# Kernel optimization log

Hardware: AMD Instinct MI355X
Metric: run time of the kernel (lower is better)

Reference implementation:

```python
import jax, jax.numpy as jnp
import numpy as np

N, E, B = 100000, 800000, 64
IN, HC1, HC2, NC, SA = 256, 128, 32, 2, 350
NEG = 0.2  # GATv2Conv default negative_slope


def forward(s_x, s_edge_index, s_batch, s_root_n_id,
            Wq, bq, Wk, bk, Wv, bv,
            Wl1, bl1, Wr1, br1, att1, bias1,
            Wl2, bl2, Wr2, br2, att2, bias2,
            Wl3, bl3, Wr3, br3, att3, bias3,
            c1w, c1b, c2W, c2b, c3W, c3b,
            linW, linb, aW1, ab1, aW2, mW1, mb1, mW2, mb2):
    src, dst = s_edge_index[0], s_edge_index[1]
    x_info = s_x
    # --- SelfAttention over seq_len=1 (x.unsqueeze(1)) ---
    z = s_x[:, None, :]                                   # [N,1,IN]
    q = z @ Wq + bq; k = z @ Wk + bk; v = z @ Wv + bv      # [N,1,SA]
    scores = jnp.einsum('nqd,nkd->nqk', q, k) / jnp.sqrt(jnp.float32(SA))
    probs = jax.nn.softmax(scores, axis=-1)
    h = jnp.einsum('nqk,nkd->nqd', probs, v)[:, 0, :]      # [N,SA]

    def gatv2(x, Wl, bl, Wr, br, att, bias):
        # PyG GATv2Conv, heads=1, eval mode (dropout off)
        xl = x @ Wl + bl                                   # source transform [N,O]
        xr = x @ Wr + br                                   # target transform [N,O]
        e = jax.nn.leaky_relu(xl[src] + xr[dst], NEG)      # [E,O]
        s = e @ att                                        # [E]
        smax = jax.ops.segment_max(s, dst, num_segments=N)
        smax = jnp.where(jnp.isfinite(smax), smax, 0.0)
        ex = jnp.exp(s - smax[dst])
        den = jax.ops.segment_sum(ex, dst, num_segments=N)
        alpha = ex / jnp.maximum(den[dst], 1e-16)
        return jax.ops.segment_sum(alpha[:, None] * xl[src], dst, num_segments=N) + bias

    h = jax.nn.relu(gatv2(h, Wl1, bl1, Wr1, br1, att1, bias1))
    h = jax.nn.relu(gatv2(h, Wl2, bl2, Wr2, br2, att2, bias2))
    h = jax.nn.relu(gatv2(h, Wl3, bl3, Wr3, br3, att3, bias3))   # [N,HC2]

    # --- readout: root node feature ++ global mean pool ---
    cnt = jax.ops.segment_sum(jnp.ones((N,), h.dtype), s_batch, num_segments=B)
    pooled = jax.ops.segment_sum(h, s_batch, num_segments=B) / jnp.maximum(cnt, 1.0)[:, None]
    sx = jnp.concatenate([h[s_root_n_id], pooled], axis=-1)       # [B,2*HC2]

    # --- info branch on raw root features ---
    info = x_info[s_root_n_id]                                    # [B,IN]
    info = c1w[0] * info[:, :-2] + c1w[1] * info[:, 1:-1] + c1w[2] * info[:, 2:] + c1b  # Conv1d(1,1,3)
    t = info.T                                                    # [IN-2,B]
    t = jax.nn.relu(c2W @ t + c2b[:, None])                       # [HC1,B]
    t = jax.nn.relu(c3W @ t + c3b[:, None])                       # [HC1//2,B]
    t = t.T                                                       # [B,HC1//2]
    L = t.shape[1]
    t = jax.nn.relu(t.reshape(B, HC2, L // HC2).mean(-1))         # AdaptiveAvgPool1d(HC2)

    sx = jax.nn.relu(sx @ linW + linb)                            # [B,HC2]

    # --- semantic attention over the two views ---
    emb = jnp.stack([sx, t], axis=1)                              # [B,2,HC2]
    w = jnp.tanh(emb @ aW1 + ab1) @ aW2                           # [B,2,1]
    beta = jax.nn.softmax(w, axis=1)
    emb = (beta * emb).sum(1)                                     # [B,HC2]

    return jax.nn.softmax(jnp.tanh(emb @ mW1 + mb1) @ mW2 + mb2, axis=1)  # [B,NC]


def setup_inputs() -> dict:
    keys = iter(jax.random.split(jax.random.key(0), 64))
    def nrm(*shape):
        return jax.random.normal(next(keys), shape, dtype=jnp.float32) * 0.05
    inp = {}
    inp['s_x'] = jax.random.normal(next(keys), (N, IN), dtype=jnp.float32)
    inp['s_edge_index'] = jax.random.randint(next(keys), (2, E), 0, N)
    inp['s_batch'] = jnp.sort(jax.random.randint(next(keys), (N,), 0, B))
    inp['s_root_n_id'] = jax.random.randint(next(keys), (B,), 0, N)
    inp['Wq'] = nrm(IN, SA); inp['bq'] = nrm(SA)
    inp['Wk'] = nrm(IN, SA); inp['bk'] = nrm(SA)
    inp['Wv'] = nrm(IN, SA); inp['bv'] = nrm(SA)
    inp['Wl1'] = nrm(SA, HC1); inp['bl1'] = nrm(HC1)
    inp['Wr1'] = nrm(SA, HC1); inp['br1'] = nrm(HC1)
    inp['att1'] = nrm(HC1); inp['bias1'] = nrm(HC1)
    inp['Wl2'] = nrm(HC1, HC1 // 2); inp['bl2'] = nrm(HC1 // 2)
    inp['Wr2'] = nrm(HC1, HC1 // 2); inp['br2'] = nrm(HC1 // 2)
    inp['att2'] = nrm(HC1 // 2); inp['bias2'] = nrm(HC1 // 2)
    inp['Wl3'] = nrm(HC1 // 2, HC2); inp['bl3'] = nrm(HC2)
    inp['Wr3'] = nrm(HC1 // 2, HC2); inp['br3'] = nrm(HC2)
    inp['att3'] = nrm(HC2); inp['bias3'] = nrm(HC2)
    inp['c1w'] = nrm(3); inp['c1b'] = nrm(1)
    inp['c2W'] = nrm(HC1, IN - 2); inp['c2b'] = nrm(HC1)
    inp['c3W'] = nrm(HC1 // 2, HC1); inp['c3b'] = nrm(HC1 // 2)
    inp['linW'] = nrm(2 * HC2, HC2); inp['linb'] = nrm(HC2)
    inp['aW1'] = nrm(HC2, 16); inp['ab1'] = nrm(16); inp['aW2'] = nrm(16, 1)
    inp['mW1'] = nrm(HC2, 16); inp['mb1'] = nrm(16)
    inp['mW2'] = nrm(16, NC); inp['mb2'] = nrm(NC)
    return inp


def reference(s_x, s_edge_index, s_batch, s_root_n_id,
              Wq, bq, Wk, bk, Wv, bv,
              Wl1, bl1, Wr1, br1, att1, bias1,
              Wl2, bl2, Wr2, br2, att2, bias2,
              Wl3, bl3, Wr3, br3, att3, bias3,
              c1w, c1b, c2W, c2b, c3W, c3b,
              linW, linb, aW1, ab1, aW2, mW1, mb1, mW2, mb2):
    return forward(s_x, s_edge_index, s_batch, s_root_n_id,
                   Wq, bq, Wk, bk, Wv, bv,
                   Wl1, bl1, Wr1, br1, att1, bias1,
                   Wl2, bl2, Wr2, br2, att2, bias2,
                   Wl3, bl3, Wr3, br3, att3, bias3,
                   c1w, c1b, c2W, c2b, c3W, c3b,
                   linW, linb, aW1, ab1, aW2, mW1, mb1, mW2, mb2)
```

## Files before the change

### kernel.cpp

```cpp
#include <hip/hip_runtime.h>
#include <hip/hip_bf16.h>
#include <math.h>

typedef unsigned short ushort_t;
typedef __attribute__((ext_vector_type(8))) short bfrag;
typedef __attribute__((ext_vector_type(4))) float ffrag;

constexpr int N_NODES = 100000;
constexpr int N_EDGES = 800000;
constexpr int NB      = 64;
constexpr int IN_F    = 256;
constexpr int HC1C    = 128;
constexpr int HC2C    = 32;
constexpr int SA_D    = 350;
constexpr float NEG   = 0.2f;

constexpr int SCAN_NBLK = (N_NODES + 255) / 256;
constexpr int MB128     = (N_NODES + 127) / 128;

constexpr size_t OFF_WT1    = 0;
constexpr size_t OFF_WT2    = OFF_WT1 + 65536;
constexpr size_t OFF_WT3    = OFF_WT2 + 16384;
constexpr size_t OFF_BC1    = OFF_WT3 + 4096;
constexpr size_t OFF_BC2    = OFF_BC1 + 256;
constexpr size_t OFF_BC3    = OFF_BC2 + 128;
constexpr size_t OFF_XLR    = OFF_BC3 + 64;
constexpr size_t OFF_H      = OFF_XLR + (size_t)N_NODES * 256;
constexpr size_t OFF_DEG    = OFF_H + (size_t)N_NODES * 128;
constexpr size_t OFF_ROWPTR = OFF_DEG + N_NODES;
constexpr size_t OFF_CURSOR = OFF_ROWPTR + N_NODES + 1;
constexpr size_t OFF_BLKS   = OFF_CURSOR + N_NODES;
constexpr size_t OFF_BLKO   = OFF_BLKS + 512;
constexpr size_t OFF_CSRSRC = OFF_BLKO + 512;
constexpr size_t OFF_POOLED = OFF_CSRSRC + N_EDGES;
constexpr size_t OFF_CNT    = OFF_POOLED + NB * HC2C;
constexpr size_t WS_FLOATS  = OFF_CNT + NB;

__device__ __forceinline__ ushort_t f2bf(float f) {
  union { float f; unsigned int u; } a;
  a.f = f;
  unsigned int r = a.u + 0x7FFFu + ((a.u >> 16) & 1u);
  return (ushort_t)(r >> 16);
}
__device__ __forceinline__ float bf2f(ushort_t h) {
  union { unsigned int u; float f; } a;
  a.u = ((unsigned int)h) << 16;
  return a.f;
}
__device__ __forceinline__ float2 bfp(unsigned int u) {
  float2 r;
  r.x = __uint_as_float(u << 16);
  r.y = __uint_as_float(u & 0xFFFF0000u);
  return r;
}
__device__ __forceinline__ unsigned int pack2(float a, float b) {
  unsigned int ua = __float_as_uint(a);
  ua += 0x7FFFu + ((ua >> 16) & 1u);
  unsigned int ub = __float_as_uint(b);
  ub += 0x7FFFu + ((ub >> 16) & 1u);
  return __builtin_amdgcn_perm(ub, ua, 0x07060302u);
}
__device__ __forceinline__ void unp8(uint4 u, float* x) {
  float2 p0 = bfp(u.x), p1 = bfp(u.y), p2 = bfp(u.z), p3 = bfp(u.w);
  x[0] = p0.x; x[1] = p0.y; x[2] = p1.x; x[3] = p1.y;
  x[4] = p2.x; x[5] = p2.y; x[6] = p3.x; x[7] = p3.y;
}

__global__ void k_pack_all(const float* __restrict__ Wv, const float* __restrict__ bv,
                           const float* __restrict__ Wl1, const float* __restrict__ bl1,
                           const float* __restrict__ Wr1, const float* __restrict__ br1,
                           const float* __restrict__ Wl2, const float* __restrict__ bl2,
                           const float* __restrict__ Wr2, const float* __restrict__ br2,
                           const float* __restrict__ Wl3, const float* __restrict__ bl3,
                           const float* __restrict__ Wr3, const float* __restrict__ br3,
                           ushort_t* __restrict__ WT1, float* __restrict__ bc1,
                           ushort_t* __restrict__ WT2, float* __restrict__ bc2,
                           ushort_t* __restrict__ WT3, float* __restrict__ bc3) {
  int blk = blockIdx.x;
  int tid = threadIdx.x;
  if (blk < 256) {
    int t = blk * 256 + tid;
    int n = t & 255, k = t >> 8;
    const float* Wx = (n < 128) ? Wl1 : Wr1;
    int j = n & 127;
    float a = 0.f;
    for (int kk = 0; kk < SA_D; ++kk) a += Wv[k * SA_D + kk] * Wx[kk * 128 + j];
    WT1[(size_t)n * 256 + k] = f2bf(a);
  } else if (blk == 256) {
    int n = tid;
    const float* Wx = (n < 128) ? Wl1 : Wr1;
    const float* bx = (n < 128) ? bl1 : br1;
    int j = n & 127;
    float a = bx[j];
    for (int kk = 0; kk < SA_D; ++kk) a += bv[kk] * Wx[kk * 128 + j];
    bc1[n] = a;
  } else if (blk < 321) {
    int t = (blk - 257) * 256 + tid;
    int n = t & 127, k = t >> 7;
    if (t < 128) bc2[t] = (t < 64) ? bl2[t] : br2[t - 64];
    float v = (n < 64) ? Wl2[k * 64 + n] : Wr2[k * 64 + (n - 64)];
    WT2[(size_t)n * 128 + k] = f2bf(v);
  } else {
    int t = (blk - 321) * 256 + tid;
    int n = t & 63, k = t >> 6;
    if (t < 64) bc3[t] = (t < 32) ? bl3[t] : br3[t - 32];
    float v = (n < 32) ? Wl3[k * 32 + n] : Wr3[k * 32 + (n - 32)];
    WT3[(size_t)n * 64 + k] = f2bf(v);
  }
}

__global__ void k_hist(const int* __restrict__ dst, int* __restrict__ deg) {
  int e = blockIdx.x * blockDim.x + threadIdx.x;
  if (e < N_EDGES) atomicAdd(deg + dst[e], 1);
}

__global__ void k_scan_local(const int* __restrict__ deg, int* __restrict__ row_ptr,
                             int* __restrict__ blk_sum) {
  __shared__ int sh[256];
  int t = threadIdx.x;
  int i = blockIdx.x * 256 + t;
  int v = (i < N_NODES) ? deg[i] : 0;
  sh[t] = v;
  __syncthreads();
  for (int off = 1; off < 256; off <<= 1) {
    int add = (t >= off) ? sh[t - off] : 0;
    __syncthreads();
    sh[t] += add;
    __syncthreads();
  }
  if (i < N_NODES) row_ptr[i] = sh[t] - v;
  if (t == 255) blk_sum[blockIdx.x] = sh[255];
}

__global__ void k_scan_blk(const int* __restrict__ blk_sum, int* __restrict__ blk_off) {
  __shared__ int sh[512];
  int t = threadIdx.x;
  int v = (t < SCAN_NBLK) ? blk_sum[t] : 0;
  sh[t] = v;
  __syncthreads();
  for (int off = 1; off < 512; off <<= 1) {
    int add = (t >= off) ? sh[t - off] : 0;
    __syncthreads();
    sh[t] += add;
    __syncthreads();
  }
  blk_off[t] = sh[t] - v;
}

__global__ void k_scan_add(int* __restrict__ row_ptr, const int* __restrict__ blk_off,
                           int* __restrict__ cursor) {
  int i = blockIdx.x * blockDim.x + threadIdx.x;
  if (i < N_NODES) {
    int v = row_ptr[i] + blk_off[i >> 8];
    row_ptr[i] = v;
    cursor[i] = v;
  }
  if (i == 0) row_ptr[N_NODES] = N_EDGES;
}

__global__ void k_fill(const int* __restrict__ src, const int* __restrict__ dst,
                       int* __restrict__ cursor, int* __restrict__ csr_src) {
  int e = blockIdx.x * blockDim.x + threadIdx.x;
  if (e >= N_EDGES) return;
  int pos = atomicAdd(cursor + dst[e], 1);
  csr_src[pos] = src[e];
}

template <int K, int NN, int BN, bool AF32>
__global__ __launch_bounds__(256) void k_gemm_bf16(const void* __restrict__ xin,
                                                   const ushort_t* __restrict__ WT,
                                                   const float* __restrict__ bc,
                                                   ushort_t* __restrict__ out, int M) {
  constexpr int BM  = 128;
  constexpr int RT  = 2;
  constexpr int CT  = BN / 16;
  constexpr int NK  = K / 32;
  constexpr int CPR = K / 8;
  __shared__ ushort_t Bs[(size_t)BN * K];

  const int tid  = threadIdx.x;
  const int wave = tid >> 6;
  const int lane = tid & 63;
  const int quad = lane >> 4;
  const int l16  = lane & 15;
  const int x7   = l16 & 7;
  const int m0   = blockIdx.x * BM;
  const int n0   = blockIdx.y * BN;

  constexpr int NCHUNK = BN * CPR;
  static_assert(NCHUNK % 256 == 0, "staging divisibility");
#pragma unroll
  for (int it = 0; it < NCHUNK / 256; ++it) {
    unsigned idx = it * 256u + tid;
    unsigned n  = idx / CPR;
    unsigned cp = idx % CPR;
    unsigned c  = cp ^ (n & 7u);
    uint4 u = *(const uint4*)(WT + (size_t)(n0 + n) * K + c * 8);
    *(uint4*)&Bs[(size_t)idx * 8] = u;
  }
  __syncthreads();

  const float*    af32 = (const float*)xin;
  const ushort_t* ab16 = (const ushort_t*)xin;
  size_t aoff[RT];
#pragma unroll
  for (int rt = 0; rt < RT; ++rt) {
    int m = m0 + wave * 32 + rt * 16 + l16;
    if (m >= M) m = M - 1;
    aoff[rt] = (size_t)m * K + quad * 8;
  }

  ffrag acc[RT][CT];
#pragma unroll
  for (int rt = 0; rt < RT; ++rt)
#pragma unroll
    for (int ct = 0; ct < CT; ++ct) acc[rt][ct] = ffrag{0.f, 0.f, 0.f, 0.f};

  float4 pf0[RT], pf1[RT];
  bfrag  pb[RT];
  if (AF32) {
#pragma unroll
    for (int rt = 0; rt < RT; ++rt) {
      pf0[rt] = *(const float4*)(af32 + aoff[rt]);
      pf1[rt] = *(const float4*)(af32 + aoff[rt] + 4);
    }
  } else {
#pragma unroll
    for (int rt = 0; rt < RT; ++rt) pb[rt] = *(const bfrag*)(ab16 + aoff[rt]);
  }

#pragma unroll
  for (int ks = 0; ks < NK; ++ks) {
    bfrag a[RT];
    if (AF32) {
#pragma unroll
      for (int rt = 0; rt < RT; ++rt) {
        uint4 d;
        d.x = pack2(pf0[rt].x, pf0[rt].y);
        d.y = pack2(pf0[rt].z, pf0[rt].w);
        d.z = pack2(pf1[rt].x, pf1[rt].y);
        d.w = pack2(pf1[rt].z, pf1[rt].w);
        a[rt] = *(bfrag*)&d;
      }
    } else {
#pragma unroll
      for (int rt = 0; rt < RT; ++rt) a[rt] = pb[rt];
    }
    if (ks + 1 < NK) {
      if (AF32) {
#pragma unroll
        for (int rt = 0; rt < RT; ++rt) {
          pf0[rt] = *(const float4*)(af32 + aoff[rt] + (ks + 1) * 32);
          pf1[rt] = *(const float4*)(af32 + aoff[rt] + (ks + 1) * 32 + 4);
        }
      } else {
#pragma unroll
        for (int rt = 0; rt < RT; ++rt)
          pb[rt] = *(const bfrag*)(ab16 + aoff[rt] + (ks + 1) * 32);
      }
    }
#pragma unroll
    for (int ct = 0; ct < CT; ++ct) {
      const int cc = (ks * 4 + quad) ^ x7;
      bfrag b = *(const bfrag*)&Bs[(size_t)(ct * 16 + l16) * K + cc * 8];
#pragma unroll
      for (int rt = 0; rt < RT; ++rt)
        acc[rt][ct] = __builtin_amdgcn_mfma_f32_16x16x32_bf16(a[rt], b, acc[rt][ct], 0, 0, 0);
    }
  }

#pragma unroll
  for (int rt = 0; rt < RT; ++rt)
#pragma unroll
    for (int ct = 0; ct < CT; ++ct) {
      const int n = n0 + ct * 16 + l16;
      const float bb = bc[n];
#pragma unroll
      for (int r = 0; r < 4; ++r) {
        const int m = m0 + wave * 32 + rt * 16 + quad * 4 + r;
        if (m < M) out[(size_t)m * NN + n] = f2bf(acc[rt][ct][r] + bb);
      }
    }
}

template <int C>
__global__ void k_gat(const ushort_t* __restrict__ xlr, const int* __restrict__ row_ptr,
                      const int* __restrict__ csr_src, const float* __restrict__ att,
                      const float* __restrict__ bias, ushort_t* __restrict__ h) {
  constexpr int G = C / 8;
  constexpr int RS = 2 * C;
  int t = blockIdx.x * blockDim.x + threadIdx.x;
  int d = t / G;
  int lane = t - d * G;
  if (d >= N_NODES) return;
  float xr[8], a[8];
  unp8(*(const uint4*)(xlr + (size_t)d * RS + C + lane * 8), xr);
  *(float4*)&a[0] = *(const float4*)(att + lane * 8);
  *(float4*)&a[4] = *(const float4*)(att + lane * 8 + 4);
  float acc[8];
#pragma unroll
  for (int j = 0; j < 8; ++j) acc[j] = 0.f;
  float den = 0.f;
  const int e0 = row_ptr[d], e1 = row_ptr[d + 1];
  int i = e0;
  for (; i + 4 <= e1; i += 4) {
    uint4 u[4];
#pragma unroll
    for (int q = 0; q < 4; ++q)
      u[q] = *(const uint4*)(xlr + (size_t)csr_src[i + q] * RS + lane * 8);
    float xl[4][8];
#pragma unroll
    for (int q = 0; q < 4; ++q) unp8(u[q], xl[q]);
    float p[4] = {0.f, 0.f, 0.f, 0.f};
#pragma unroll
    for (int j = 0; j < 8; ++j) {
#pragma unroll
      for (int q = 0; q < 4; ++q) {
        float v = xl[q][j] + xr[j];
        v = v > 0.f ? v : NEG * v;
        p[q] += a[j] * v;
      }
    }
#pragma unroll
    for (int off = G / 2; off > 0; off >>= 1) {
#pragma unroll
      for (int q = 0; q < 4; ++q) p[q] += __shfl_xor(p[q], off, 64);
    }
    float ex[4];
#pragma unroll
    for (int q = 0; q < 4; ++q) ex[q] = expf(p[q]);
    den += (ex[0] + ex[1]) + (ex[2] + ex[3]);
#pragma unroll
    for (int j = 0; j < 8; ++j)
      acc[j] += (ex[0] * xl[0][j] + ex[1] * xl[1][j]) + (ex[2] * xl[2][j] + ex[3] * xl[3][j]);
  }
  for (; i < e1; ++i) {
    int s = csr_src[i];
    float xl[8];
    unp8(*(const uint4*)(xlr + (size_t)s * RS + lane * 8), xl);
    float p = 0.f;
#pragma unroll
    for (int j = 0; j < 8; ++j) {
      float v = xl[j] + xr[j];
      v = v > 0.f ? v : NEG * v;
      p += a[j] * v;
    }
#pragma unroll
    for (int off = G / 2; off > 0; off >>= 1) p += __shfl_xor(p, off, 64);
    float ex = expf(p);
    den += ex;
#pragma unroll
    for (int j = 0; j < 8; ++j) acc[j] += ex * xl[j];
  }
  float inv = 1.f / fmaxf(den, 1e-16f);
  float o[8];
#pragma unroll
  for (int j = 0; j < 8; ++j)
    o[j] = fmaxf(acc[j] * inv + bias[lane * 8 + j], 0.f);
  uint4 pk;
  pk.x = pack2(o[0], o[1]);
  pk.y = pack2(o[2], o[3]);
  pk.z = pack2(o[4], o[5]);
  pk.w = pack2(o[6], o[7]);
  *(uint4*)(h + (size_t)d * C + lane * 8) = pk;
}

__global__ void k_pool(const ushort_t* __restrict__ h3, const int* __restrict__ batch,
                       float* __restrict__ pooled, float* __restrict__ cnt) {
  constexpr int NPB = 1024;
  constexpr int NPT = NPB / 8;
  int c = threadIdx.x & 31;
  int r = threadIdx.x >> 5;
  int base = blockIdx.x * NPB + r * NPT;
  if (base >= N_NODES) return;
  int end = base + NPT;
  if (end > N_NODES) end = N_NODES;
  int cur_b = batch[base];
  float acc = 0.f, count = 0.f;
  for (int n = base; n < end; ++n) {
    int b = batch[n];
    if (b != cur_b) {
      atomicAdd(pooled + cur_b * HC2C + c, acc);
      if (c == 0) atomicAdd(cnt + cur_b, count);
      cur_b = b;
      acc = 0.f;
      count = 0.f;
    }
    acc += bf2f(h3[(size_t)n * HC2C + c]);
    count += 1.f;
  }
  atomicAdd(pooled + cur_b * HC2C + c, acc);
  if (c == 0) atomicAdd(cnt + cur_b, count);
}

__global__ __launch_bounds__(256) void k_tail(
    const ushort_t* __restrict__ h3, const int* __restrict__ root,
    const float* __restrict__ pooled, const float* __restrict__ cnt,
    const float* __restrict__ linW, const float* __restrict__ linb,
    const float* __restrict__ X, const float* __restrict__ c1w,
    const float* __restrict__ c1b, const float* __restrict__ c2W,
    const float* __restrict__ c2b, const float* __restrict__ c3W,
    const float* __restrict__ c3b, const float* __restrict__ aW1,
    const float* __restrict__ ab1, const float* __restrict__ aW2,
    const float* __restrict__ mW1, const float* __restrict__ mb1,
    const float* __restrict__ mW2, const float* __restrict__ mb2,
    float* __restrict__ out) {
  constexpr int L = IN_F - 2;
  __shared__ float s_info[L];
  __shared__ float s_t1[HC1C];
  __shared__ float s_t2[HC1C / 2];
  __shared__ float s_e0[HC2C];
  __shared__ float s_e1[HC2C];
  const int b = blockIdx.x;
  const int tid = threadIdx.x;
  const int r = root[b];
  const float* xr = X + (size_t)r * IN_F;
  for (int i = tid; i < L; i += 256)
    s_info[i] = c1w[0] * xr[i] + c1w[1] * xr[i + 1] + c1w[2] * xr[i + 2] + c1b[0];
  __syncthreads();
  if (tid < HC1C) {
    float a = c2b[tid];
    for (int i = 0; i < L; ++i) a += c2W[tid * L + i] * s_info[i];
    s_t1[tid] = fmaxf(a, 0.f);
  }
  __syncthreads();
  if (tid < HC1C / 2) {
    float a = c3b[tid];
    for (int i = 0; i < HC1C; ++i) a += c3W[tid * HC1C + i] * s_t1[i];
    s_t2[tid] = fmaxf(a, 0.f);
  }
  __syncthreads();
  if (tid < HC2C) {
    float v = 0.5f * (s_t2[2 * tid] + s_t2[2 * tid + 1]);
    s_e1[tid] = fmaxf(v, 0.f);
  } else if (tid < 2 * HC2C) {
    int j = tid - HC2C;
    float inv = 1.f / fmaxf(cnt[b], 1.f);
    float a = linb[j];
    for (int c = 0; c < HC2C; ++c) a += bf2f(h3[(size_t)r * HC2C + c]) * linW[c * HC2C + j];
    for (int c = 0; c < HC2C; ++c) a += pooled[b * HC2C + c] * inv * linW[(HC2C + c) * HC2C + j];
    s_e0[j] = fmaxf(a, 0.f);
  }
  __syncthreads();
  if (tid == 0) {
    float w0 = 0.f, w1 = 0.f;
    for (int j = 0; j < 16; ++j) {
      float z0 = ab1[j], z1 = ab1[j];
      for (int c = 0; c < HC2C; ++c) {
        z0 += s_e0[c] * aW1[c * 16 + j];
        z1 += s_e1[c] * aW1[c * 16 + j];
      }
      w0 += tanhf(z0) * aW2[j];
      w1 += tanhf(z1) * aW2[j];
    }
    float mx = fmaxf(w0, w1);
    float x0 = expf(w0 - mx), x1 = expf(w1 - mx);
    float inv = 1.f / (x0 + x1);
    float b0 = x0 * inv, b1 = x1 * inv;
    float l0 = mb2[0], l1 = mb2[1];
    for (int j = 0; j < 16; ++j) {
      float z = mb1[j];
      for (int c = 0; c < HC2C; ++c) z += (b0 * s_e0[c] + b1 * s_e1[c]) * mW1[c * 16 + j];
      float tz = tanhf(z);
      l0 += tz * mW2[j * 2 + 0];
      l1 += tz * mW2[j * 2 + 1];
    }
    float m2 = fmaxf(l0, l1);
    float y0 = expf(l0 - m2), y1 = expf(l1 - m2);
    float is = 1.f / (y0 + y1);
    out[b * 2 + 0] = y0 * is;
    out[b * 2 + 1] = y1 * is;
  }
}

extern "C" void kernel_launch(void* const* d_in, const int* in_sizes, int n_in, void* d_out,
                              int out_size, void* d_ws, size_t ws_size, hipStream_t stream) {
  if (ws_size < WS_FLOATS * sizeof(float)) return;

  const float* s_x   = (const float*)d_in[0];
  const int*   edge  = (const int*)d_in[1];
  const int*   batch = (const int*)d_in[2];
  const int*   root  = (const int*)d_in[3];
  const float* Wv    = (const float*)d_in[8];
  const float* bv    = (const float*)d_in[9];
  const float* Wl1   = (const float*)d_in[10];
  const float* bl1   = (const float*)d_in[11];
  const float* Wr1   = (const float*)d_in[12];
  const float* br1   = (const float*)d_in[13];
  const float* att1  = (const float*)d_in[14];
  const float* bias1 = (const float*)d_in[15];
  const float* Wl2   = (const float*)d_in[16];
  const float* bl2   = (const float*)d_in[17];
  const float* Wr2   = (const float*)d_in[18];
  const float* br2   = (const float*)d_in[19];
  const float* att2  = (const float*)d_in[20];
  const float* bias2 = (const float*)d_in[21];
  const float* Wl3   = (const float*)d_in[22];
  const float* bl3   = (const float*)d_in[23];
  const float* Wr3   = (const float*)d_in[24];
  const float* br3   = (const float*)d_in[25];
  const float* att3  = (const float*)d_in[26];
  const float* bias3 = (const float*)d_in[27];
  const float* c1w   = (const float*)d_in[28];
  const float* c1b   = (const float*)d_in[29];
  const float* c2W   = (const float*)d_in[30];
  const float* c2b   = (const float*)d_in[31];
  const float* c3W   = (const float*)d_in[32];
  const float* c3b   = (const float*)d_in[33];
  const float* linW  = (const float*)d_in[34];
  const float* linb  = (const float*)d_in[35];
  const float* aW1   = (const float*)d_in[36];
  const float* ab1   = (const float*)d_in[37];
  const float* aW2   = (const float*)d_in[38];
  const float* mW1   = (const float*)d_in[39];
  const float* mb1   = (const float*)d_in[40];
  const float* mW2   = (const float*)d_in[41];
  const float* mb2   = (const float*)d_in[42];

  const int* src = edge;
  const int* dst = edge + N_EDGES;

  float*    ws      = (float*)d_ws;
  ushort_t* WT1     = (ushort_t*)(ws + OFF_WT1);
  ushort_t* WT2     = (ushort_t*)(ws + OFF_WT2);
  ushort_t* WT3     = (ushort_t*)(ws + OFF_WT3);
  float*    bc1     = ws + OFF_BC1;
  float*    bc2     = ws + OFF_BC2;
  float*    bc3     = ws + OFF_BC3;
  ushort_t* xlr     = (ushort_t*)(ws + OFF_XLR);
  ushort_t* hbuf    = (ushort_t*)(ws + OFF_H);
  int*      deg     = (int*)(ws + OFF_DEG);
  int*      row_ptr = (int*)(ws + OFF_ROWPTR);
  int*      cursor  = (int*)(ws + OFF_CURSOR);
  int*      blks    = (int*)(ws + OFF_BLKS);
  int*      blko    = (int*)(ws + OFF_BLKO);
  int*      csr_src = (int*)(ws + OFF_CSRSRC);
  float*    pooled  = ws + OFF_POOLED;
  float*    cnt     = ws + OFF_CNT;
  float*    out     = (float*)d_out;

  hipMemsetAsync(deg, 0, N_NODES * sizeof(int), stream);
  k_hist<<<(N_EDGES + 255) / 256, 256, 0, stream>>>(dst, deg);
  k_scan_local<<<SCAN_NBLK, 256, 0, stream>>>(deg, row_ptr, blks);
  k_scan_blk<<<1, 512, 0, stream>>>(blks, blko);
  k_scan_add<<<SCAN_NBLK, 256, 0, stream>>>(row_ptr, blko, cursor);
  k_fill<<<(N_EDGES + 255) / 256, 256, 0, stream>>>(src, dst, cursor, csr_src);

  k_pack_all<<<337, 256, 0, stream>>>(Wv, bv, Wl1, bl1, Wr1, br1, Wl2, bl2, Wr2, br2, Wl3,
                                      bl3, Wr3, br3, WT1, bc1, WT2, bc2, WT3, bc3);

  k_gemm_bf16<256, 256, 128, true><<<dim3(MB128, 2), 256, 0, stream>>>(s_x, WT1, bc1, xlr,
                                                                       N_NODES);
  k_gat<128><<<(N_NODES * 16 + 255) / 256, 256, 0, stream>>>(xlr, row_ptr, csr_src, att1,
                                                             bias1, hbuf);

  k_gemm_bf16<128, 128, 128, false><<<dim3(MB128, 1), 256, 0, stream>>>(hbuf, WT2, bc2, xlr,
                                                                        N_NODES);
  k_gat<64><<<(N_NODES * 8 + 255) / 256, 256, 0, stream>>>(xlr, row_ptr, csr_src, att2,
                                                           bias2, hbuf);

  k_gemm_bf16<64, 64, 64, false><<<dim3(MB128, 1), 256, 0, stream>>>(hbuf, WT3, bc3, xlr,
                                                                     N_NODES);
  k_gat<32><<<(N_NODES * 4 + 255) / 256, 256, 0, stream>>>(xlr, row_ptr, csr_src, att3,
                                                           bias3, hbuf);

  hipMemsetAsync(pooled, 0, (NB * HC2C + NB) * sizeof(float), stream);
  k_pool<<<(N_NODES + 1023) / 1024, 256, 0, stream>>>(hbuf, batch, pooled, cnt);
  k_tail<<<NB, 256, 0, stream>>>(hbuf, root, pooled, cnt, linW, linb, s_x, c1w, c1b, c2W,
                                 c2b, c3W, c3b, aW1, ab1, aW2, mW1, mb1, mW2, mb2, out);
}
```

Before: 643.8 us.

## Double-buffer GEMM A/B tiles in LDS via direct global-to-LDS loads

The bf16 MFMA GEMM used to stage the full weight slab into LDS once and stream A straight from global into registers. It now stages both the A and B k-slices (32 wide) into double-buffered LDS with global_load_lds, using XOR-swizzled layouts, and prefetches the next slice while computing the current one. This aims to hide global load latency and cut LDS footprint and register pressure. It adds a barrier per k-step, and the swizzle and index math must match the load_lds lane-to-address mapping.

Result: faster. 630.1 us (-2.1%).

```diff
diff --git a/kernel.cpp b/kernel.cpp
--- a/kernel.cpp
+++ b/kernel.cpp
@@ -5,6 +5,9 @@
 typedef unsigned short ushort_t;
 typedef __attribute__((ext_vector_type(8))) short bfrag;
 typedef __attribute__((ext_vector_type(4))) float ffrag;
+
+#define GLOBAL_AS __attribute__((address_space(1)))
+#define LDS_AS    __attribute__((address_space(3)))
 
 constexpr int N_NODES = 100000;
 constexpr int N_EDGES = 800000;
@@ -171,101 +174,104 @@
                                                    const ushort_t* __restrict__ WT,
                                                    const float* __restrict__ bc,
                                                    ushort_t* __restrict__ out, int M) {
-  constexpr int BM  = 128;
-  constexpr int RT  = 2;
-  constexpr int CT  = BN / 16;
-  constexpr int NK  = K / 32;
-  constexpr int CPR = K / 8;
-  __shared__ ushort_t Bs[(size_t)BN * K];
+  constexpr int BM     = 128;
+  constexpr int RT     = 2;
+  constexpr int CT     = BN / 16;
+  constexpr int NK     = K / 32;
+  constexpr int ABYTES = AF32 ? BM * 32 * 4 : BM * 32 * 2;
+  constexpr int BBYTES = BN * 32 * 2;
+  constexpr int AG     = ABYTES / 16;
+  constexpr int BG     = BBYTES / 16;
+  constexpr int NG     = AG + BG;
+  static_assert(NG % 256 == 0, "staging divisibility");
+  static_assert(AG % 256 == 0, "A/B chunk straddle");
+  __shared__ __align__(16) ushort_t lds[2][(ABYTES + BBYTES) / 2];
 
   const int tid  = threadIdx.x;
   const int wave = tid >> 6;
   const int lane = tid & 63;
   const int quad = lane >> 4;
   const int l16  = lane & 15;
-  const int x7   = l16 & 7;
   const int m0   = blockIdx.x * BM;
   const int n0   = blockIdx.y * BN;
 
-  constexpr int NCHUNK = BN * CPR;
-  static_assert(NCHUNK % 256 == 0, "staging divisibility");
-#pragma unroll
-  for (int it = 0; it < NCHUNK / 256; ++it) {
-    unsigned idx = it * 256u + tid;
-    unsigned n  = idx / CPR;
-    unsigned cp = idx % CPR;
-    unsigned c  = cp ^ (n & 7u);
-    uint4 u = *(const uint4*)(WT + (size_t)(n0 + n) * K + c * 8);
-    *(uint4*)&Bs[(size_t)idx * 8] = u;
-  }
-  __syncthreads();
-
   const float*    af32 = (const float*)xin;
   const ushort_t* ab16 = (const ushort_t*)xin;
-  size_t aoff[RT];
-#pragma unroll
-  for (int rt = 0; rt < RT; ++rt) {
-    int m = m0 + wave * 32 + rt * 16 + l16;
-    if (m >= M) m = M - 1;
-    aoff[rt] = (size_t)m * K + quad * 8;
-  }
-
-  ffrag acc[RT][CT];
-#pragma unroll
-  for (int rt = 0; rt < RT; ++rt)
-#pragma unroll
-    for (int ct = 0; ct < CT; ++ct) acc[rt][ct] = ffrag{0.f, 0.f, 0.f, 0.f};
-
-  float4 pf0[RT], pf1[RT];
-  bfrag  pb[RT];
-  if (AF32) {
-#pragma unroll
-    for (int rt = 0; rt < RT; ++rt) {
-      pf0[rt] = *(const float4*)(af32 + aoff[rt]);
-      pf1[rt] = *(const float4*)(af32 + aoff[rt] + 4);
-    }
-  } else {
-#pragma unroll
-    for (int rt = 0; rt < RT; ++rt) pb[rt] = *(const bfrag*)(ab16 + aoff[rt]);
-  }
-
-#pragma unroll
-  for (int ks = 0; ks < NK; ++ks) {
-    bfrag a[RT];
-    if (AF32) {
-#pragma unroll
-      for (int rt = 0; rt < RT; ++rt) {
-        uint4 d;
-        d.x = pack2(pf0[rt].x, pf0[rt].y);
-        d.y = pack2(pf0[rt].z, pf0[rt].w);
-        d.z = pack2(pf1[rt].x, pf1[rt].y);
-        d.w = pack2(pf1[rt].z, pf1[rt].w);
-        a[rt] = *(bfrag*)&d;
-      }
-    } else {
-#pragma unroll
-      for (int rt = 0; rt < RT; ++rt) a[rt] = pb[rt];
-    }
-    if (ks + 1 < NK) {
-      if (AF32) {
-#pragma unroll
-        for (int rt = 0; rt < RT; ++rt) {
-          pf0[rt] = *(const float4*)(af32 + aoff[rt] + (ks + 1) * 32);
-          pf1[rt] = *(const float4*)(af32 + aoff[rt] + (ks + 1) * 32 + 4);
+
+  auto stage = [&](int ks, int b) {
+#pragma unroll
+    for (int it = 0; it < NG / 256; ++it) {
+      const int s = it * 256 + tid;
+      const void* src;
+      if (s < AG) {
+        const int line  = s >> 3;
+        const int inner = (s & 7) ^ (line & 7);
+        if (AF32) {
+          int m = m0 + line;
+          if (m >= M) m = M - 1;
+          src = (const void*)(af32 + (size_t)m * K + ks * 32 + inner * 4);
+        } else {
+          const int row = line * 2 + (inner >> 2);
+          int m = m0 + row;
+          if (m >= M) m = M - 1;
+          src = (const void*)(ab16 + (size_t)m * K + ks * 32 + (inner & 3) * 8);
         }
       } else {
-#pragma unroll
-        for (int rt = 0; rt < RT; ++rt)
-          pb[rt] = *(const bfrag*)(ab16 + aoff[rt] + (ks + 1) * 32);
+        const int sb    = s - AG;
+        const int line  = sb >> 3;
+        const int inner = (sb & 7) ^ (line & 7);
+        const int n     = line * 2 + (inner >> 2);
+        src = (const void*)(WT + (size_t)(n0 + n) * K + ks * 32 + (inner & 3) * 8);
       }
+      ushort_t* dst = &lds[b][(size_t)(it * 256 + wave * 64) * 8];
+      __builtin_amdgcn_global_load_lds((const GLOBAL_AS unsigned int*)src,
+                                       (LDS_AS unsigned int*)dst, 16, 0, 0);
+    }
+  };
+
+  ffrag acc[RT][CT];
+#pragma unroll
+  for (int rt = 0; rt < RT; ++rt)
+#pragma unroll
+    for (int ct = 0; ct < CT; ++ct) acc[rt][ct] = ffrag{0.f, 0.f, 0.f, 0.f};
+
+  stage(0, 0);
+
+#pragma unroll
+  for (int ks = 0; ks < NK; ++ks) {
+    const int b = ks & 1;
+    __syncthreads();
+    if (ks + 1 < NK) stage(ks + 1, b ^ 1);
+
+    bfrag a[RT];
+#pragma unroll
+    for (int rt = 0; rt < RT; ++rt) {
+      const int row = wave * 32 + rt * 16 + l16;
+      if (AF32) {
+        const int x = l16 & 7;
+        const float4 u0 = *(const float4*)&lds[b][((size_t)row * 8 + ((quad * 2) ^ x)) * 8];
+        const float4 u1 = *(const float4*)&lds[b][((size_t)row * 8 + ((quad * 2 + 1) ^ x)) * 8];
+        uint4 d;
+        d.x = pack2(u0.x, u0.y);
+        d.y = pack2(u0.z, u0.w);
+        d.z = pack2(u1.x, u1.y);
+        d.w = pack2(u1.z, u1.w);
+        a[rt] = *(bfrag*)&d;
+      } else {
+        const int line  = row >> 1;
+        const int g     = ((row & 1) * 4 + quad) ^ (line & 7);
+        a[rt] = *(const bfrag*)&lds[b][((size_t)line * 8 + g) * 8];
+      }
     }
 #pragma unroll
     for (int ct = 0; ct < CT; ++ct) {
-      const int cc = (ks * 4 + quad) ^ x7;
-      bfrag b = *(const bfrag*)&Bs[(size_t)(ct * 16 + l16) * K + cc * 8];
+      const int n    = ct * 16 + l16;
+      const int line = n >> 1;
+      const int g    = ((n & 1) * 4 + quad) ^ (line & 7);
+      bfrag bfr = *(const bfrag*)&lds[b][(size_t)(AG + line * 8 + g) * 8];
 #pragma unroll
       for (int rt = 0; rt < RT; ++rt)
-        acc[rt][ct] = __builtin_amdgcn_mfma_f32_16x16x32_bf16(a[rt], b, acc[rt][ct], 0, 0, 0);
+        acc[rt][ct] = __builtin_amdgcn_mfma_f32_16x16x32_bf16(a[rt], bfr, acc[rt][ct], 0, 0, 0);
     }
   }
 
```

## Stage activation tiles in LDS and stream weights from registers in GEMMs

Applied to the files above, without the earlier changes.

The GEMM kernel is restructured so that the 64-row activation tile is staged in swizzled LDS instead of the weight tile. For bf16 inputs the staging uses direct global-to-LDS loads, and weight fragments are read from global/L2 with a one-step register prefetch. The block tile shrinks to 64 rows, the four waves are arranged as 2x2, and the launch bound asks for 4 blocks per CU to raise occupancy. The trade-off is more repeated weight reads from cache and more blocks, in exchange for less LDS traffic for the large activation matrix and better latency hiding.

New measurement: 659.4 us. 1.02x slower.

```diff
diff --git a/kernel.cpp b/kernel.cpp
--- a/kernel.cpp
+++ b/kernel.cpp
@@ -5,6 +5,9 @@
 typedef unsigned short ushort_t;
 typedef __attribute__((ext_vector_type(8))) short bfrag;
 typedef __attribute__((ext_vector_type(4))) float ffrag;
+
+#define GLOBAL_AS __attribute__((address_space(1)))
+#define LDS_AS    __attribute__((address_space(3)))
 
 constexpr int N_NODES = 100000;
 constexpr int N_EDGES = 800000;
@@ -16,7 +19,7 @@
 constexpr float NEG   = 0.2f;
 
 constexpr int SCAN_NBLK = (N_NODES + 255) / 256;
-constexpr int MB128     = (N_NODES + 127) / 128;
+constexpr int MB64      = (N_NODES + 63) / 64;
 
 constexpr size_t OFF_WT1    = 0;
 constexpr size_t OFF_WT2    = OFF_WT1 + 65536;
@@ -167,47 +170,67 @@
 }
 
 template <int K, int NN, int BN, bool AF32>
-__global__ __launch_bounds__(256) void k_gemm_bf16(const void* __restrict__ xin,
-                                                   const ushort_t* __restrict__ WT,
-                                                   const float* __restrict__ bc,
-                                                   ushort_t* __restrict__ out, int M) {
-  constexpr int BM  = 128;
+__global__ __launch_bounds__(256, 4) void k_gemm_bf16(const void* __restrict__ xin,
+                                                      const ushort_t* __restrict__ WT,
+                                                      const float* __restrict__ bc,
+                                                      ushort_t* __restrict__ out, int M) {
+  constexpr int BM  = 64;
   constexpr int RT  = 2;
-  constexpr int CT  = BN / 16;
+  constexpr int CT  = BN / 32;
   constexpr int NK  = K / 32;
-  constexpr int CPR = K / 8;
-  __shared__ ushort_t Bs[(size_t)BN * K];
+  constexpr int GPR = K / 8;
+  __shared__ __align__(16) ushort_t As[BM * K];
 
   const int tid  = threadIdx.x;
   const int wave = tid >> 6;
   const int lane = tid & 63;
   const int quad = lane >> 4;
   const int l16  = lane & 15;
-  const int x7   = l16 & 7;
+  const int wrow = wave & 1;
+  const int wcol = wave >> 1;
   const int m0   = blockIdx.x * BM;
   const int n0   = blockIdx.y * BN;
-
-  constexpr int NCHUNK = BN * CPR;
-  static_assert(NCHUNK % 256 == 0, "staging divisibility");
-#pragma unroll
-  for (int it = 0; it < NCHUNK / 256; ++it) {
-    unsigned idx = it * 256u + tid;
-    unsigned n  = idx / CPR;
-    unsigned cp = idx % CPR;
-    unsigned c  = cp ^ (n & 7u);
-    uint4 u = *(const uint4*)(WT + (size_t)(n0 + n) * K + c * 8);
-    *(uint4*)&Bs[(size_t)idx * 8] = u;
-  }
-  __syncthreads();
+  const int nb   = n0 + wcol * (BN / 2);
 
   const float*    af32 = (const float*)xin;
   const ushort_t* ab16 = (const ushort_t*)xin;
-  size_t aoff[RT];
-#pragma unroll
-  for (int rt = 0; rt < RT; ++rt) {
-    int m = m0 + wave * 32 + rt * 16 + l16;
-    if (m >= M) m = M - 1;
-    aoff[rt] = (size_t)m * K + quad * 8;
+
+  bfrag bcur[CT], bnxt[CT];
+#pragma unroll
+  for (int ct = 0; ct < CT; ++ct)
+    bcur[ct] = *(const bfrag*)(WT + (size_t)(nb + ct * 16 + l16) * K + quad * 8);
+
+  if (AF32) {
+    float4 av[16];
+#pragma unroll
+    for (int j = 0; j < 16; ++j) {
+      const int r = wave * 16 + j;
+      int m = m0 + r;
+      if (m >= M) m = M - 1;
+      av[j] = *(const float4*)(af32 + (size_t)m * K + lane * 4);
+    }
+#pragma unroll
+    for (int j = 0; j < 16; ++j) {
+      const int r = wave * 16 + j;
+      uint2 pk;
+      pk.x = pack2(av[j].x, av[j].y);
+      pk.y = pack2(av[j].z, av[j].w);
+      *(uint2*)&As[(size_t)r * K + (((lane >> 1) ^ (r & 7)) * 8) + (lane & 1) * 4] = pk;
+    }
+  } else {
+    constexpr int NI = GPR / 4;
+#pragma unroll
+    for (int j = 0; j < NI; ++j) {
+      const int s0 = (wave * NI + j) * 64;
+      const int s  = s0 + lane;
+      const int r  = s / GPR;
+      const int c  = s & (GPR - 1);
+      int m = m0 + r;
+      if (m >= M) m = M - 1;
+      const ushort_t* srcp = ab16 + (size_t)m * K + (size_t)(c ^ (r & 7)) * 8;
+      __builtin_amdgcn_global_load_lds((const GLOBAL_AS unsigned int*)srcp,
+                                       (LDS_AS unsigned int*)&As[(size_t)s0 * 8], 16, 0, 0);
+    }
   }
 
   ffrag acc[RT][CT];
@@ -216,68 +239,41 @@
 #pragma unroll
     for (int ct = 0; ct < CT; ++ct) acc[rt][ct] = ffrag{0.f, 0.f, 0.f, 0.f};
 
-  float4 pf0[RT], pf1[RT];
-  bfrag  pb[RT];
-  if (AF32) {
+  __syncthreads();
+
+#pragma unroll
+  for (int ks = 0; ks < NK; ++ks) {
+    if (ks + 1 < NK) {
+#pragma unroll
+      for (int ct = 0; ct < CT; ++ct)
+        bnxt[ct] = *(const bfrag*)(WT + (size_t)(nb + ct * 16 + l16) * K + (ks + 1) * 32 + quad * 8);
+    }
+    bfrag a[RT];
 #pragma unroll
     for (int rt = 0; rt < RT; ++rt) {
-      pf0[rt] = *(const float4*)(af32 + aoff[rt]);
-      pf1[rt] = *(const float4*)(af32 + aoff[rt] + 4);
-    }
-  } else {
-#pragma unroll
-    for (int rt = 0; rt < RT; ++rt) pb[rt] = *(const bfrag*)(ab16 + aoff[rt]);
-  }
-
-#pragma unroll
-  for (int ks = 0; ks < NK; ++ks) {
-    bfrag a[RT];
-    if (AF32) {
-#pragma unroll
-      for (int rt = 0; rt < RT; ++rt) {
-        uint4 d;
-        d.x = pack2(pf0[rt].x, pf0[rt].y);
-        d.y = pack2(pf0[rt].z, pf0[rt].w);
-        d.z = pack2(pf1[rt].x, pf1[rt].y);
-        d.w = pack2(pf1[rt].z, pf1[rt].w);
-        a[rt] = *(bfrag*)&d;
-      }
-    } else {
-#pragma unroll
-      for (int rt = 0; rt < RT; ++rt) a[rt] = pb[rt];
-    }
+      const int r = wrow * 32 + rt * 16 + l16;
+      a[rt] = *(const bfrag*)&As[(size_t)r * K + (size_t)(((ks * 4 + quad) ^ (r & 7)) * 8)];
+    }
+#pragma unroll
+    for (int ct = 0; ct < CT; ++ct)
+#pragma unroll
+      for (int rt = 0; rt < RT; ++rt)
+        acc[rt][ct] = __builtin_amdgcn_mfma_f32_16x16x32_bf16(a[rt], bcur[ct], acc[rt][ct], 0, 0, 0);
     if (ks + 1 < NK) {
-      if (AF32) {
-#pragma unroll
-        for (int rt = 0; rt < RT; ++rt) {
-          pf0[rt] = *(const float4*)(af32 + aoff[rt] + (ks + 1) * 32);
-          pf1[rt] = *(const float4*)(af32 + aoff[rt] + (ks + 1) * 32 + 4);
-        }
-      } else {
-#pragma unroll
-        for (int rt = 0; rt < RT; ++rt)
-          pb[rt] = *(const bfrag*)(ab16 + aoff[rt] + (ks + 1) * 32);
-      }
-    }
+#pragma unroll
+      for (int ct = 0; ct < CT; ++ct) bcur[ct] = bnxt[ct];
+    }
+  }
+
+#pragma unroll
+  for (int rt = 0; rt < RT; ++rt)
 #pragma unroll
     for (int ct = 0; ct < CT; ++ct) {
-      const int cc = (ks * 4 + quad) ^ x7;
-      bfrag b = *(const bfrag*)&Bs[(size_t)(ct * 16 + l16) * K + cc * 8];
-#pragma unroll
-      for (int rt = 0; rt < RT; ++rt)
-        acc[rt][ct] = __builtin_amdgcn_mfma_f32_16x16x32_bf16(a[rt], b, acc[rt][ct], 0, 0, 0);
-    }
-  }
-
-#pragma unroll
-  for (int rt = 0; rt < RT; ++rt)
-#pragma unroll
-    for (int ct = 0; ct < CT; ++ct) {
-      const int n = n0 + ct * 16 + l16;
+      const int n = nb + ct * 16 + l16;
       const float bb = bc[n];
 #pragma unroll
       for (int r = 0; r < 4; ++r) {
-        const int m = m0 + wave * 32 + rt * 16 + quad * 4 + r;
+        const int m = m0 + wrow * 32 + rt * 16 + quad * 4 + r;
         if (m < M) out[(size_t)m * NN + n] = f2bf(acc[rt][ct][r] + bb);
       }
     }
@@ -549,18 +545,18 @@
   k_pack_all<<<337, 256, 0, stream>>>(Wv, bv, Wl1, bl1, Wr1, br1, Wl2, bl2, Wr2, br2, Wl3,
                                       bl3, Wr3, br3, WT1, bc1, WT2, bc2, WT3, bc3);
 
-  k_gemm_bf16<256, 256, 128, true><<<dim3(MB128, 2), 256, 0, stream>>>(s_x, WT1, bc1, xlr,
-                                                                       N_NODES);
+  k_gemm_bf16<256, 256, 128, true><<<dim3(MB64, 2), 256, 0, stream>>>(s_x, WT1, bc1, xlr,
+                                                                      N_NODES);
   k_gat<128><<<(N_NODES * 16 + 255) / 256, 256, 0, stream>>>(xlr, row_ptr, csr_src, att1,
                                                              bias1, hbuf);
 
-  k_gemm_bf16<128, 128, 128, false><<<dim3(MB128, 1), 256, 0, stream>>>(hbuf, WT2, bc2, xlr,
-                                                                        N_NODES);
+  k_gemm_bf16<128, 128, 128, false><<<dim3(MB64, 1), 256, 0, stream>>>(hbuf, WT2, bc2, xlr,
+                                                                       N_NODES);
   k_gat<64><<<(N_NODES * 8 + 255) / 256, 256, 0, stream>>>(xlr, row_ptr, csr_src, att2,
                                                            bias2, hbuf);
 
-  k_gemm_bf16<64, 64, 64, false><<<dim3(MB128, 1), 256, 0, stream>>>(hbuf, WT3, bc3, xlr,
-                                                                     N_NODES);
+  k_gemm_bf16<64, 64, 64, false><<<dim3(MB64, 1), 256, 0, stream>>>(hbuf, WT3, bc3, xlr,
+                                                                    N_NODES);
   k_gat<32><<<(N_NODES * 4 + 255) / 256, 256, 0, stream>>>(xlr, row_ptr, csr_src, att3,
                                                            bias3, hbuf);
 
```
